# Optimization experiments

Hardware: AMD Instinct MI355X
Metric: run time of the kernel (lower is better)

Reference implementation:

```python
import jax, jax.numpy as jnp
import numpy as np

N_KERNELS = 5
MUL_FACTOR = 2.0
# 2.0 ** (arange(5) - 2) = [0.25, 0.5, 1, 2, 4]
BANDWIDTH_MULTIPLIERS = MUL_FACTOR ** (np.arange(N_KERNELS) - N_KERNELS // 2)


def setup_inputs() -> dict:
    key = jax.random.key(0)
    kx, ky = jax.random.split(key)
    X = jax.random.normal(kx, (4096, 256), dtype=jnp.float32)
    Y = jax.random.normal(ky, (4096, 256), dtype=jnp.float32)
    return {"X": X, "Y": Y}


def _pairwise_sq_dists(Z):
    # ||z_i - z_j||^2 via GEMM; clamp tiny negatives from roundoff.
    sq = jnp.sum(Z * Z, axis=-1)  # [2N]
    d2 = sq[:, None] + sq[None, :] - 2.0 * (Z @ Z.T)  # [2N, 2N]
    return jnp.maximum(d2, 0.0)


def reference(X, Y):
    n = X.shape[0]
    Z = jnp.concatenate([X, Y], axis=0)  # [2N, D]
    d2 = _pairwise_sq_dists(Z)  # [2N, 2N]
    n_samples = d2.shape[0]
    # bandwidth uses .data in torch -> detached
    bandwidth = jax.lax.stop_gradient(d2.sum()) / (n_samples ** 2 - n_samples)
    mults = jnp.asarray(BANDWIDTH_MULTIPLIERS, dtype=d2.dtype)  # [5]
    # K = sum_k exp(-d2 / (bandwidth * mult_k))
    K = jnp.exp(-d2[None, :, :] / (bandwidth * mults)[:, None, None]).sum(axis=0)
    XX = K[:n, :n].mean()
    XY = K[:n, n:].mean()
    YY = K[n:, n:].mean()
    return XX - 2.0 * XY + YY
```

## Files before the change

### kernel.cpp

```cpp
#include <hip/hip_runtime.h>
#include <math.h>


#define N_HALF 4096
#define DIM 256
#define M_TOT 8192
#define TILE 128
#define NT 64
#define NT_HALF 32
#define CHUNK 4
#define NCHUNK 520

typedef unsigned short ushort_t;
typedef __attribute__((ext_vector_type(8))) short short8;
typedef __attribute__((ext_vector_type(4))) float floatx4;

__device__ ushort_t g_zf[M_TOT * DIM];

__device__ __forceinline__ ushort_t f2bf(float f) {
    unsigned u = __float_as_uint(f);
    u += 0x7fffu + ((u >> 16) & 1u);
    return (ushort_t)(u >> 16);
}

__device__ __forceinline__ void load_frags(const ushort_t* aP, const ushort_t* bP,
                                           int kk, short8 (&af)[4], short8 (&bf)[4]) {
#pragma unroll
    for (int mi = 0; mi < 4; ++mi)
        af[mi] = *(const short8*)(aP + (size_t)mi * 4096 + kk * 512);
#pragma unroll
    for (int ni = 0; ni < 4; ++ni)
        bf[ni] = *(const short8*)(bP + (size_t)ni * 4096 + kk * 512);
}

__device__ __forceinline__ void mfma16(const short8 (&af)[4], const short8 (&bf)[4],
                                       floatx4 (&accv)[4][4]) {
#pragma unroll
    for (int mi = 0; mi < 4; ++mi)
#pragma unroll
        for (int ni = 0; ni < 4; ++ni)
            accv[mi][ni] = __builtin_amdgcn_mfma_f32_16x16x32_bf16(
                af[mi], bf[ni], accv[mi][ni], 0, 0, 0);
}

__global__ __launch_bounds__(256) void k_prep(const float* __restrict__ X,
                                              const float* __restrict__ Y,
                                              float* __restrict__ sq,
                                              float* __restrict__ colsum_r,
                                              float* __restrict__ Ssum_r) {
    __shared__ float cpart[4][256];
    __shared__ float spart[4];
    const int t = threadIdx.x, wave = t >> 6, lane = t & 63;
    const int row0 = blockIdx.x * 64 + wave * 16;
    const int kk = lane >> 3, q = (lane >> 1) & 3, j0 = (lane & 1) * 4;
    float c0 = 0.f, c1 = 0.f, c2 = 0.f, c3 = 0.f, ssum = 0.f;
#pragma unroll 4
    for (int i = 0; i < 16; ++i) {
        const int row = row0 + i;
        const float* p = (row < N_HALF) ? (X + (size_t)row * DIM)
                                        : (Y + (size_t)(row - N_HALF) * DIM);
        const float4 v = *((const float4*)p + lane);
        ushort4 hi;
        hi.x = f2bf(v.x); hi.y = f2bf(v.y); hi.z = f2bf(v.z); hi.w = f2bf(v.w);
        const int rb = row >> 4, m = row & 15;
        *(ushort4*)(g_zf + (size_t)rb * 4096 + kk * 512 + m * 32 + q * 8 + j0) = hi;
        c0 += v.x; c1 += v.y; c2 += v.z; c3 += v.w;
        float s = fmaf(v.x, v.x, fmaf(v.y, v.y, fmaf(v.z, v.z, v.w * v.w)));
#pragma unroll
        for (int off = 32; off > 0; off >>= 1) s += __shfl_xor(s, off);
        if (lane == 0) sq[row] = s;
        ssum += s;
    }
    float4 cp; cp.x = c0; cp.y = c1; cp.z = c2; cp.w = c3;
    *(float4*)&cpart[wave][lane * 4] = cp;
    if (lane == 0) spart[wave] = ssum;
    __syncthreads();
    const float cs = cpart[0][t] + cpart[1][t] + cpart[2][t] + cpart[3][t];
    const int rep = blockIdx.x & 7;
    atomicAdd(&colsum_r[rep * 256 + t], cs);
    if (t == 0) atomicAdd(&Ssum_r[rep], spart[0] + spart[1] + spart[2] + spart[3]);
}

__global__ __launch_bounds__(256) void k_gram(const float* __restrict__ sq,
                                              const float* __restrict__ colsum_r,
                                              const float* __restrict__ Ssum_r,
                                              double* __restrict__ acc,
                                              unsigned* __restrict__ cnt,
                                              float* __restrict__ out) {
    const int bid = (int)blockIdx.x;
    const int cc = (bid & 7) * 65 + (bid >> 3);
    const int f0 = cc * CHUNK;

    __shared__ double redw[4][3];

    const int t = threadIdx.x;
    const int lane = t & 63, wave = t >> 6;
    const int l15 = lane & 15, quad = lane >> 4;
    const int wrow = (wave >> 1) * 64, wcol = (wave & 1) * 64;

    {
        float csf = 0.f;
#pragma unroll
        for (int r = 0; r < 8; ++r) csf += colsum_r[r * 256 + t];
        double p = (double)csf * (double)csf;
#pragma unroll
        for (int off = 32; off > 0; off >>= 1) p += __shfl_xor(p, off);
        if (lane == 0) redw[wave][0] = p;
    }
    __syncthreads();
    const double SS = redw[0][0] + redw[1][0] + redw[2][0] + redw[3][0];
    float Sf = 0.f;
#pragma unroll
    for (int r = 0; r < 8; ++r) Sf += Ssum_r[r];
    const double sum_d2 = 2.0 * (double)M_TOT * (double)Sf - 2.0 * SS;
    const double bw = sum_d2 / ((double)M_TOT * (double)M_TOT - (double)M_TOT);
    const float c2 = (float)(1.4426950408889634 / (4.0 * bw));
    const float twoc2 = 2.f * c2;
    __syncthreads();

    int ti = (int)((129.0f - sqrtf(16641.0f - 8.0f * (float)f0)) * 0.5f);
    if (ti < 0) ti = 0; if (ti > NT - 1) ti = NT - 1;
    while (ti * NT - ti * (ti - 1) / 2 > f0) --ti;
    while ((ti + 1) * NT - (ti + 1) * ti / 2 <= f0) ++ti;
    int tj = ti + (f0 - (ti * NT - ti * (ti - 1) / 2));

    const int laneoff = l15 * 32 + quad * 8;
    const ushort_t* aP = g_zf + (size_t)((ti * TILE + wrow) >> 4) * 4096 + laneoff;
    const ushort_t* bP = g_zf + (size_t)((tj * TILE + wcol) >> 4) * 4096 + laneoff;

    short8 af0[4], bf0[4], af1[4], bf1[4];
    load_frags(aP, bP, 0, af0, bf0);

    double lxx = 0.0, lxy = 0.0, lyy = 0.0;

#pragma unroll
    for (int s = 0; s < CHUNK; ++s) {
        floatx4 accv[4][4];
#pragma unroll
        for (int mi = 0; mi < 4; ++mi)
#pragma unroll
            for (int ni = 0; ni < 4; ++ni) accv[mi][ni] = (floatx4)0.f;

#pragma unroll
        for (int kk = 0; kk < 8; kk += 2) {
            load_frags(aP, bP, kk + 1, af1, bf1);
            mfma16(af0, bf0, accv);
            if (kk + 2 < 8) load_frags(aP, bP, kk + 2, af0, bf0);
            mfma16(af1, bf1, accv);
        }

        const int cti = ti, ctj = tj;
        if (s < CHUNK - 1) {
            ++tj; if (tj == NT) { ++ti; tj = ti; }
            aP = g_zf + (size_t)((ti * TILE + wrow) >> 4) * 4096 + laneoff;
            bP = g_zf + (size_t)((tj * TILE + wcol) >> 4) * 4096 + laneoff;
            load_frags(aP, bP, 0, af0, bf0);
        }

        const int arow0 = cti * TILE, brow0 = ctj * TILE;
        float nsj[4];
#pragma unroll
        for (int ni = 0; ni < 4; ++ni)
            nsj[ni] = -c2 * sq[brow0 + wcol + ni * 16 + l15];
        floatx4 nsi4[4];
#pragma unroll
        for (int mi = 0; mi < 4; ++mi) {
            const float4 sv = *(const float4*)&sq[arow0 + wrow + mi * 16 + quad * 4];
            nsi4[mi][0] = -c2 * sv.x; nsi4[mi][1] = -c2 * sv.y;
            nsi4[mi][2] = -c2 * sv.z; nsi4[mi][3] = -c2 * sv.w;
        }
        floatx4 sum4 = (floatx4)0.f;
#pragma unroll
        for (int mi = 0; mi < 4; ++mi) {
#pragma unroll
            for (int ni = 0; ni < 4; ++ni) {
                const floatx4 addv = nsi4[mi] + (floatx4)nsj[ni];
                floatx4 arg = twoc2 * accv[mi][ni] + addv;
                floatx4 tt;
#pragma unroll
                for (int r = 0; r < 4; ++r) tt[r] = exp2f(fminf(arg[r], 0.f));
                const floatx4 t2 = tt * tt, t4 = t2 * t2, t8 = t4 * t4, t16 = t8 * t8;
                sum4 += (tt + t2) + (t4 + t8) + t16;
            }
        }
        const float fsum = (sum4[0] + sum4[1]) + (sum4[2] + sum4[3]);
        const double contrib = ((cti == ctj) ? 1.0 : 2.0) * (double)fsum;
        if (ctj < NT_HALF)       lxx += contrib;
        else if (cti < NT_HALF)  lxy += contrib;
        else                     lyy += contrib;
    }

#pragma unroll
    for (int off = 32; off > 0; off >>= 1) {
        lxx += __shfl_xor(lxx, off);
        lxy += __shfl_xor(lxy, off);
        lyy += __shfl_xor(lyy, off);
    }
    if (lane == 0) { redw[wave][0] = lxx; redw[wave][1] = lxy; redw[wave][2] = lyy; }
    __syncthreads();
    if (t == 0) {
        double sxx = 0.0, sxy = 0.0, syy = 0.0;
#pragma unroll
        for (int wv = 0; wv < 4; ++wv) {
            sxx += redw[wv][0]; sxy += redw[wv][1]; syy += redw[wv][2];
        }
        if (sxx != 0.0) atomicAdd(&acc[0], sxx);
        if (sxy != 0.0) atomicAdd(&acc[1], sxy);
        if (syy != 0.0) atomicAdd(&acc[2], syy);
        __threadfence();
        const unsigned old = atomicAdd(cnt, 1u);
        if (old == (0xAAAAAAAAu + (unsigned)(NCHUNK - 1)) ||
            old == (unsigned)(NCHUNK - 1)) {
            const double xx = atomicAdd(&acc[0], 0.0);
            const double xy = atomicAdd(&acc[1], 0.0);
            const double yy = atomicAdd(&acc[2], 0.0);
            out[0] = (float)((xx + yy - xy) *
                             (1.0 / ((double)N_HALF * (double)N_HALF)));
        }
    }
}

extern "C" void kernel_launch(void* const* d_in, const int* in_sizes, int n_in,
                              void* d_out, int out_size, void* d_ws, size_t ws_size,
                              hipStream_t stream) {
    const float* X = (const float*)d_in[0];
    const float* Y = (const float*)d_in[1];
    char* ws = (char*)d_ws;
    float* sq        = (float*)ws;
    float* colsum_r  = (float*)(ws + 32768);
    float* Ssum_r    = (float*)(ws + 40960);
    unsigned* cnt    = (unsigned*)(ws + 40992);
    double* acc      = (double*)(ws + 41000);
    float* out = (float*)d_out;

    hipLaunchKernelGGL(k_prep, dim3(128), dim3(256), 0, stream,
                       X, Y, sq, colsum_r, Ssum_r);
    hipLaunchKernelGGL(k_gram, dim3(NCHUNK), dim3(256), 0, stream,
                       sq, colsum_r, Ssum_r, acc, cnt, out);
}
```

Measured before the change: 137.0 us.

## Stage B tile in LDS via global_load_lds instead of per-wave global loads

The B operand tile (128 rows x 256 dims, bf16) is now copied into shared memory with asynchronous global-to-LDS loads, and waves read their B fragments from LDS. A fragments still come from global memory. This halves redundant global/L2 traffic for B, since two waves previously fetched the same B columns. In exchange it adds two block barriers per tile and a 64KB LDS allocation that may reduce occupancy. The next tile's load is issued during the epilogue, so there is some overlap.

```diff
diff --git a/kernel.cpp b/kernel.cpp
--- a/kernel.cpp
+++ b/kernel.cpp
@@ -23,14 +23,18 @@
     return (ushort_t)(u >> 16);
 }
 
-__device__ __forceinline__ void load_frags(const ushort_t* aP, const ushort_t* bP,
-                                           int kk, short8 (&af)[4], short8 (&bf)[4]) {
+__device__ __forceinline__ void load_afrags(const ushort_t* aP, int kk,
+                                            short8 (&af)[4]) {
 #pragma unroll
     for (int mi = 0; mi < 4; ++mi)
         af[mi] = *(const short8*)(aP + (size_t)mi * 4096 + kk * 512);
+}
+
+__device__ __forceinline__ void read_bfrags(const ushort_t* Bs, int bfb, int kk,
+                                            short8 (&bf)[4]) {
 #pragma unroll
     for (int ni = 0; ni < 4; ++ni)
-        bf[ni] = *(const short8*)(bP + (size_t)ni * 4096 + kk * 512);
+        bf[ni] = *(const short8*)(Bs + bfb + ni * 4096 + kk * 512);
 }
 
 __device__ __forceinline__ void mfma16(const short8 (&af)[4], const short8 (&bf)[4],
@@ -87,11 +91,12 @@
                                               double* __restrict__ acc,
                                               unsigned* __restrict__ cnt,
                                               float* __restrict__ out) {
+    __shared__ __align__(16) ushort_t Bs[TILE * DIM];
+    __shared__ double redw[4][3];
+
     const int bid = (int)blockIdx.x;
     const int cc = (bid & 7) * 65 + (bid >> 3);
     const int f0 = cc * CHUNK;
-
-    __shared__ double redw[4][3];
 
     const int t = threadIdx.x;
     const int lane = t & 63, wave = t >> 6;
@@ -125,36 +130,58 @@
     int tj = ti + (f0 - (ti * NT - ti * (ti - 1) / 2));
 
     const int laneoff = l15 * 32 + quad * 8;
-    const ushort_t* aP = g_zf + (size_t)((ti * TILE + wrow) >> 4) * 4096 + laneoff;
-    const ushort_t* bP = g_zf + (size_t)((tj * TILE + wcol) >> 4) * 4096 + laneoff;
-
-    short8 af0[4], bf0[4], af1[4], bf1[4];
-    load_frags(aP, bP, 0, af0, bf0);
+    const int bfb = (wcol >> 4) * 4096 + laneoff;
+    const ushort_t* aP = g_zf + (size_t)(ti * 8 + (wrow >> 4)) * 4096 + laneoff;
+
+#pragma unroll
+    for (int i = 0; i < 16; ++i) {
+        const int e = wave * 16 + i;
+        __builtin_amdgcn_global_load_lds(
+            (const __attribute__((address_space(1))) void*)
+                (g_zf + (size_t)tj * 32768 + e * 512 + lane * 8),
+            (__attribute__((address_space(3))) void*)(Bs + e * 512), 16, 0, 0);
+    }
 
     double lxx = 0.0, lxy = 0.0, lyy = 0.0;
 
 #pragma unroll
     for (int s = 0; s < CHUNK; ++s) {
+        __syncthreads();
+
         floatx4 accv[4][4];
 #pragma unroll
         for (int mi = 0; mi < 4; ++mi)
 #pragma unroll
             for (int ni = 0; ni < 4; ++ni) accv[mi][ni] = (floatx4)0.f;
 
+        short8 af0[4], af1[4], bf0[4], bf1[4];
+        load_afrags(aP, 0, af0);
+        read_bfrags(Bs, bfb, 0, bf0);
 #pragma unroll
         for (int kk = 0; kk < 8; kk += 2) {
-            load_frags(aP, bP, kk + 1, af1, bf1);
+            load_afrags(aP, kk + 1, af1);
+            read_bfrags(Bs, bfb, kk + 1, bf1);
             mfma16(af0, bf0, accv);
-            if (kk + 2 < 8) load_frags(aP, bP, kk + 2, af0, bf0);
+            if (kk + 2 < 8) {
+                load_afrags(aP, kk + 2, af0);
+                read_bfrags(Bs, bfb, kk + 2, bf0);
+            }
             mfma16(af1, bf1, accv);
         }
 
         const int cti = ti, ctj = tj;
+        __syncthreads();
         if (s < CHUNK - 1) {
             ++tj; if (tj == NT) { ++ti; tj = ti; }
-            aP = g_zf + (size_t)((ti * TILE + wrow) >> 4) * 4096 + laneoff;
-            bP = g_zf + (size_t)((tj * TILE + wcol) >> 4) * 4096 + laneoff;
-            load_frags(aP, bP, 0, af0, bf0);
+            aP = g_zf + (size_t)(ti * 8 + (wrow >> 4)) * 4096 + laneoff;
+#pragma unroll
+            for (int i = 0; i < 16; ++i) {
+                const int e = wave * 16 + i;
+                __builtin_amdgcn_global_load_lds(
+                    (const __attribute__((address_space(1))) void*)
+                        (g_zf + (size_t)tj * 32768 + e * 512 + lane * 8),
+                    (__attribute__((address_space(3))) void*)(Bs + e * 512), 16, 0, 0);
+            }
         }
 
         const int arow0 = cti * TILE, brow0 = ctj * TILE;
```

After: 139.6 us. No clear change (+1.8%).

## Replicate bf16 operand buffer per XCD, halve chunk size, split bandwidth kernel

Applied to the files above, without the earlier changes.

The prep kernel now writes eight copies of the bf16 swizzled Z buffer, and each gram block reads the copy indexed by blockIdx&7. This is meant to give each XCD its own L2-local copy and avoid cross-die traffic. Chunk size drops from 4 to 2 tiles, doubling the block count to 1040 for better load balance. The bandwidth constant is now computed in a separate one-block kernel, so gram blocks no longer each do the reduction and two syncthreads. In exchange, prep writes eight times as much data and there is an extra kernel launch.

```diff
diff --git a/kernel.cpp b/kernel.cpp
--- a/kernel.cpp
+++ b/kernel.cpp
@@ -8,14 +8,14 @@
 #define TILE 128
 #define NT 64
 #define NT_HALF 32
-#define CHUNK 4
-#define NCHUNK 520
+#define CHUNK 2
+#define NCHUNK 1040
 
 typedef unsigned short ushort_t;
 typedef __attribute__((ext_vector_type(8))) short short8;
 typedef __attribute__((ext_vector_type(4))) float floatx4;
 
-__device__ ushort_t g_zf[M_TOT * DIM];
+__device__ ushort_t g_zf[8][M_TOT * DIM];
 
 __device__ __forceinline__ ushort_t f2bf(float f) {
     unsigned u = __float_as_uint(f);
@@ -63,11 +63,14 @@
         ushort4 hi;
         hi.x = f2bf(v.x); hi.y = f2bf(v.y); hi.z = f2bf(v.z); hi.w = f2bf(v.w);
         const int rb = row >> 4, m = row & 15;
-        *(ushort4*)(g_zf + (size_t)rb * 4096 + kk * 512 + m * 32 + q * 8 + j0) = hi;
+        const size_t off = (size_t)rb * 4096 + kk * 512 + m * 32 + q * 8 + j0;
+#pragma unroll
+        for (int c = 0; c < 8; ++c)
+            *(ushort4*)(&g_zf[c][off]) = hi;
         c0 += v.x; c1 += v.y; c2 += v.z; c3 += v.w;
         float s = fmaf(v.x, v.x, fmaf(v.y, v.y, fmaf(v.z, v.z, v.w * v.w)));
 #pragma unroll
-        for (int off = 32; off > 0; off >>= 1) s += __shfl_xor(s, off);
+        for (int o = 32; o > 0; o >>= 1) s += __shfl_xor(s, o);
         if (lane == 0) sq[row] = s;
         ssum += s;
     }
@@ -81,14 +84,38 @@
     if (t == 0) atomicAdd(&Ssum_r[rep], spart[0] + spart[1] + spart[2] + spart[3]);
 }
 
+__global__ __launch_bounds__(256) void k_bw(const float* __restrict__ colsum_r,
+                                            const float* __restrict__ Ssum_r,
+                                            float* __restrict__ cconst) {
+    __shared__ double red[4];
+    const int t = threadIdx.x, lane = t & 63, wave = t >> 6;
+    float csf = 0.f;
+#pragma unroll
+    for (int r = 0; r < 8; ++r) csf += colsum_r[r * 256 + t];
+    double p = (double)csf * (double)csf;
+#pragma unroll
+    for (int o = 32; o > 0; o >>= 1) p += __shfl_xor(p, o);
+    if (lane == 0) red[wave] = p;
+    __syncthreads();
+    if (t == 0) {
+        const double SS = red[0] + red[1] + red[2] + red[3];
+        float Sf = 0.f;
+#pragma unroll
+        for (int r = 0; r < 8; ++r) Sf += Ssum_r[r];
+        const double sum_d2 = 2.0 * (double)M_TOT * (double)Sf - 2.0 * SS;
+        const double bw = sum_d2 / ((double)M_TOT * (double)M_TOT - (double)M_TOT);
+        cconst[0] = (float)(1.4426950408889634 / (4.0 * bw));
+    }
+}
+
 __global__ __launch_bounds__(256) void k_gram(const float* __restrict__ sq,
-                                              const float* __restrict__ colsum_r,
-                                              const float* __restrict__ Ssum_r,
+                                              const float* __restrict__ cconst,
                                               double* __restrict__ acc,
                                               unsigned* __restrict__ cnt,
                                               float* __restrict__ out) {
     const int bid = (int)blockIdx.x;
-    const int cc = (bid & 7) * 65 + (bid >> 3);
+    const ushort_t* zf = g_zf[bid & 7];
+    const int cc = (bid & 7) * 130 + (bid >> 3);
     const int f0 = cc * CHUNK;
 
     __shared__ double redw[4][3];
@@ -98,25 +125,8 @@
     const int l15 = lane & 15, quad = lane >> 4;
     const int wrow = (wave >> 1) * 64, wcol = (wave & 1) * 64;
 
-    {
-        float csf = 0.f;
-#pragma unroll
-        for (int r = 0; r < 8; ++r) csf += colsum_r[r * 256 + t];
-        double p = (double)csf * (double)csf;
-#pragma unroll
-        for (int off = 32; off > 0; off >>= 1) p += __shfl_xor(p, off);
-        if (lane == 0) redw[wave][0] = p;
-    }
-    __syncthreads();
-    const double SS = redw[0][0] + redw[1][0] + redw[2][0] + redw[3][0];
-    float Sf = 0.f;
-#pragma unroll
-    for (int r = 0; r < 8; ++r) Sf += Ssum_r[r];
-    const double sum_d2 = 2.0 * (double)M_TOT * (double)Sf - 2.0 * SS;
-    const double bw = sum_d2 / ((double)M_TOT * (double)M_TOT - (double)M_TOT);
-    const float c2 = (float)(1.4426950408889634 / (4.0 * bw));
+    const float c2 = cconst[0];
     const float twoc2 = 2.f * c2;
-    __syncthreads();
 
     int ti = (int)((129.0f - sqrtf(16641.0f - 8.0f * (float)f0)) * 0.5f);
     if (ti < 0) ti = 0; if (ti > NT - 1) ti = NT - 1;
@@ -125,8 +135,8 @@
     int tj = ti + (f0 - (ti * NT - ti * (ti - 1) / 2));
 
     const int laneoff = l15 * 32 + quad * 8;
-    const ushort_t* aP = g_zf + (size_t)((ti * TILE + wrow) >> 4) * 4096 + laneoff;
-    const ushort_t* bP = g_zf + (size_t)((tj * TILE + wcol) >> 4) * 4096 + laneoff;
+    const ushort_t* aP = zf + (size_t)(ti * 8 + (wrow >> 4)) * 4096 + laneoff;
+    const ushort_t* bP = zf + (size_t)(tj * 8 + (wcol >> 4)) * 4096 + laneoff;
 
     short8 af0[4], bf0[4], af1[4], bf1[4];
     load_frags(aP, bP, 0, af0, bf0);
@@ -152,8 +162,8 @@
         const int cti = ti, ctj = tj;
         if (s < CHUNK - 1) {
             ++tj; if (tj == NT) { ++ti; tj = ti; }
-            aP = g_zf + (size_t)((ti * TILE + wrow) >> 4) * 4096 + laneoff;
-            bP = g_zf + (size_t)((tj * TILE + wcol) >> 4) * 4096 + laneoff;
+            aP = zf + (size_t)(ti * 8 + (wrow >> 4)) * 4096 + laneoff;
+            bP = zf + (size_t)(tj * 8 + (wcol >> 4)) * 4096 + laneoff;
             load_frags(aP, bP, 0, af0, bf0);
         }
 
@@ -231,10 +241,13 @@
     float* Ssum_r    = (float*)(ws + 40960);
     unsigned* cnt    = (unsigned*)(ws + 40992);
     double* acc      = (double*)(ws + 41000);
+    float* cconst    = (float*)(ws + 41024);
     float* out = (float*)d_out;
 
     hipLaunchKernelGGL(k_prep, dim3(128), dim3(256), 0, stream,
                        X, Y, sq, colsum_r, Ssum_r);
+    hipLaunchKernelGGL(k_bw, dim3(1), dim3(256), 0, stream,
+                       colsum_r, Ssum_r, cconst);
     hipLaunchKernelGGL(k_gram, dim3(NCHUNK), dim3(256), 0, stream,
-                       sq, colsum_r, Ssum_r, acc, cnt, out);
-}
+                       sq, cconst, acc, cnt, out);
+}
```

Measured after the change: 148.8 us. +8.6%, slower.
